# Kernel tuning notes

Measured on AMD Instinct MI355X. Metric: run time of the kernel, lower is better.

## Reference

```python
import jax, jax.numpy as jnp
import numpy as np

NUM_T = 1000      # diffusion timesteps
TIME_DIM = 16     # gaussian time embedding size
DIST_DIM = 16     # gaussian distance embedding size


def _gsmear(x, stop, num_g):
    # GaussianSmearing with linearly spaced centers in [0, stop]
    offsets = jnp.linspace(0.0, stop, num_g)
    coeff = -0.5 / (offsets[1] - offsets[0]) ** 2
    return jnp.exp(coeff * (x[:, None] - offsets[None, :]) ** 2)


def setup_inputs():
    key = jax.random.key(0)
    ks = jax.random.split(key, 20)
    N, EH, G = 20000, 100000, 1000          # nodes, halfedges, graphs
    NT, ND, ED, L, NE = 16, 256, 128, 2, 5   # node types, node_dim, edge_dim, blocks, edge types
    h_node = jax.nn.one_hot(jax.random.randint(ks[0], (N,), 0, NT), NT, dtype=jnp.float32)
    pos_node = jax.random.normal(ks[1], (N, 3), dtype=jnp.float32) * 3.0
    batch_node = jnp.sort(jax.random.randint(ks[2], (N,), 0, G))
    half = jax.random.randint(ks[3], (2, EH), 0, N)
    edge_index = jnp.concatenate([half, half[::-1]], axis=1)  # halfedges + flipped
    bh = jnp.sort(jax.random.randint(ks[4], (EH,), 0, G))
    batch_edge = jnp.concatenate([bh, bh], axis=0)
    t = jax.random.randint(ks[5], (G,), 0, NUM_T)

    def w(k, shape):
        fan_in = shape[-2] if len(shape) > 1 else shape[-1]
        return jax.random.normal(k, shape, dtype=jnp.float32) / np.sqrt(fan_in)

    e_in = ED + 2 * ND + DIST_DIM + 1
    return {
        'h_node': h_node, 'pos_node': pos_node, 'batch_node': batch_node,
        'edge_index': edge_index, 'batch_edge': batch_edge, 't': t,
        'W_node_emb': w(ks[6], (NT, ND - TIME_DIM)),
        'W_edge_emb': w(ks[7], (2 * NT, ED - TIME_DIM)),
        'We1': w(ks[8], (L, e_in, ED)), 'be1': jnp.zeros((L, ED), jnp.float32),
        'We2': w(ks[9], (L, ED, ED)), 'be2': jnp.zeros((L, ED), jnp.float32),
        'Wm': w(ks[10], (L, ND + ED, ND)), 'bm': jnp.zeros((L, ND), jnp.float32),
        'Wn1': w(ks[11], (L, 2 * ND + 1, ND)), 'bn1': jnp.zeros((L, ND), jnp.float32),
        'Wn2': w(ks[12], (L, ND, ND)), 'bn2': jnp.zeros((L, ND), jnp.float32),
        'Wd1': w(ks[13], (ED + ND, ED)), 'bd1': jnp.zeros((ED,), jnp.float32),
        'Wd2': w(ks[14], (ED, ED)), 'bd2': jnp.zeros((ED,), jnp.float32),
        'Wd3': w(ks[15], (ED, NE)), 'bd3': jnp.zeros((NE,), jnp.float32),
    }


def reference(h_node, pos_node, batch_node, edge_index, batch_edge, t,
              W_node_emb, W_edge_emb, We1, be1, We2, be2, Wm, bm,
              Wn1, bn1, Wn2, bn2, Wd1, bd1, Wd2, bd2, Wd3, bd3):
    src, dst = edge_index[0], edge_index[1]
    N = h_node.shape[0]
    L = We1.shape[0]

    # edge input features: concat of endpoint node features (gather)
    h_e0 = jnp.concatenate([h_node[src], h_node[dst]], axis=-1)

    tn = t[batch_node].astype(jnp.float32)  # per-node timestep
    te = t[batch_edge].astype(jnp.float32)  # per-edge timestep
    # linear embed + gaussian-smeared time embedding
    h_n = jnp.concatenate([h_node @ W_node_emb, _gsmear(tn, float(NUM_T), TIME_DIM)], axis=-1)
    h_e = jnp.concatenate([h_e0 @ W_edge_emb, _gsmear(te, float(NUM_T), TIME_DIM)], axis=-1)
    node_time = (tn / NUM_T)[:, None]
    edge_time = (te / NUM_T)[:, None]

    # geometric edge features
    d = jnp.linalg.norm(pos_node[dst] - pos_node[src], axis=-1)
    dist_emb = _gsmear(d, 10.0, DIST_DIM)

    # NodeEdgeNet: alternating edge / node residual updates
    for l in range(L):
        e_in = jnp.concatenate([h_e, h_n[src], h_n[dst], dist_emb, edge_time], axis=-1)
        h_e = h_e + jax.nn.relu(e_in @ We1[l] + be1[l]) @ We2[l] + be2[l]
        msg = jax.nn.relu(jnp.concatenate([h_n[src], h_e], axis=-1) @ Wm[l] + bm[l])
        agg = jax.ops.segment_sum(msg, dst, num_segments=N)
        n_in = jnp.concatenate([h_n, agg, node_time], axis=-1)
        h_n = h_n + jax.nn.relu(n_in @ Wn1[l] + bn1[l]) @ Wn2[l] + bn2[l]

    # symmetrize halfedges and decode edge types
    nh = h_e.shape[0] // 2
    h_ext = jnp.concatenate([h_e[:nh] + h_e[nh:],
                             h_n[src[:nh]] + h_n[dst[:nh]]], axis=-1)
    h = jax.nn.relu(h_ext @ Wd1 + bd1)
    h = jax.nn.relu(h @ Wd2 + bd2)
    return h @ Wd3 + bd3
```

## Files before the change

### kernel.cpp

```cpp
#include <hip/hip_runtime.h>
#include <math.h>


typedef __attribute__((ext_vector_type(8)))  short bf16x8;
typedef __attribute__((ext_vector_type(16))) float f32x16;

__device__ __forceinline__ float b2f(unsigned short u) {
    union { float f; unsigned int i; } x; x.i = ((unsigned int)u) << 16; return x.f;
}
__device__ __forceinline__ unsigned short f2b(float f) {
    union { float f; unsigned int i; } x; x.f = f;
    unsigned int r = x.i + 0x7fffu + ((x.i >> 16) & 1u);
    return (unsigned short)(r >> 16);
}
__device__ __forceinline__ bf16x8 ld8(const unsigned short* p) { return *(const bf16x8*)p; }
__device__ __forceinline__ bf16x8 zero8() { bf16x8 r = {0,0,0,0,0,0,0,0}; return r; }
__device__ __forceinline__ bf16x8 add8(bf16x8 a, bf16x8 b) {
    bf16x8 r;
#pragma unroll
    for (int j = 0; j < 8; j++) r[j] = (short)f2b(b2f((unsigned short)a[j]) + b2f((unsigned short)b[j]));
    return r;
}

#define MFMA4(ACC, A0, A1, B0, B1)                                                   \
    ACC[0][0] = __builtin_amdgcn_mfma_f32_32x32x16_bf16(A0, B0, ACC[0][0], 0, 0, 0); \
    ACC[0][1] = __builtin_amdgcn_mfma_f32_32x32x16_bf16(A0, B1, ACC[0][1], 0, 0, 0); \
    ACC[1][0] = __builtin_amdgcn_mfma_f32_32x32x16_bf16(A1, B0, ACC[1][0], 0, 0, 0); \
    ACC[1][1] = __builtin_amdgcn_mfma_f32_32x32x16_bf16(A1, B1, ACC[1][1], 0, 0, 0);

#define LANE_SETUP()                                  \
    const int tid  = threadIdx.x;                     \
    const int lane = tid & 63;                        \
    const int wave = tid >> 6;                        \
    const int wm = wave >> 1, wn = wave & 1;          \
    const int l31 = lane & 31, l5 = lane >> 5;        \
    (void)wm; (void)wn; (void)lane;

#define PIPELINE4(NITER, FETCH, ACC)                                  \
    {                                                                 \
        bf16x8 pa0[2], pb0[2], pa1[2], pb1[2], pa2[2], pb2[2];        \
        FETCH(0, pa0, pb0);                                           \
        if (1 < (NITER)) FETCH(1, pa1, pb1);                          \
        _Pragma("unroll")                                             \
        for (int i = 0; i < (NITER); i++) {                           \
            if (i + 2 < (NITER)) FETCH(i + 2, pa2, pb2);              \
            MFMA4(ACC, pa0[0], pa0[1], pb0[0], pb0[1]);               \
            pa0[0] = pa1[0]; pa0[1] = pa1[1];                         \
            pb0[0] = pb1[0]; pb0[1] = pb1[1];                         \
            pa1[0] = pa2[0]; pa1[1] = pa2[1];                         \
            pb1[0] = pb2[0]; pb1[1] = pb2[1];                         \
        }                                                             \
    }

#define PIPELINE2(NITER, FETCH, ACC)                                  \
    {                                                                 \
        bf16x8 pa0, pb0[2], pa1, pb1[2], pa2, pb2[2];                 \
        FETCH(0, pa0, pb0);                                           \
        if (1 < (NITER)) FETCH(1, pa1, pb1);                          \
        _Pragma("unroll")                                             \
        for (int i = 0; i < (NITER); i++) {                           \
            if (i + 2 < (NITER)) FETCH(i + 2, pa2, pb2);              \
            ACC[0] = __builtin_amdgcn_mfma_f32_32x32x16_bf16(pa0, pb0[0], ACC[0], 0, 0, 0); \
            ACC[1] = __builtin_amdgcn_mfma_f32_32x32x16_bf16(pa0, pb0[1], ACC[1], 0, 0, 0); \
            pa0 = pa1; pb0[0] = pb1[0]; pb0[1] = pb1[1];              \
            pa1 = pa2; pb1[0] = pb2[0]; pb1[1] = pb2[1];              \
        }                                                             \
    }

#define STAGED_COMPUTE(As, Bs, ACC)                                         \
    _Pragma("unroll")                                                       \
    for (int s = 0; s < 4; s++) {                                           \
        const int ks  = s * 2 + l5;                                         \
        const int ra0 = wm * 64 + l31, ra1 = ra0 + 32;                      \
        const int ca0 = wn * 64 + l31, ca1 = ca0 + 32;                      \
        bf16x8 a0 = *(const bf16x8*)&As[ra0][ks ^ (ra0 & 7)][0];            \
        bf16x8 a1 = *(const bf16x8*)&As[ra1][ks ^ (ra1 & 7)][0];            \
        bf16x8 b0 = *(const bf16x8*)&Bs[ca0][ks ^ (ca0 & 7)][0];            \
        bf16x8 b1 = *(const bf16x8*)&Bs[ca1][ks ^ (ca1 & 7)][0];            \
        MFMA4(ACC, a0, a1, b0, b1);                                         \
    }

__global__ void zero_i32_k(int* p, int n) {
    int i = blockIdx.x * 256 + threadIdx.x;
    if (i < n) p[i] = 0;
}
__global__ void hist_k(const int* __restrict__ dst, int* __restrict__ cnt, int E) {
    int e = blockIdx.x * 256 + threadIdx.x;
    if (e < E) atomicAdd(&cnt[dst[e]], 1);
}
__global__ __launch_bounds__(256) void scan_k(int* __restrict__ cnt, int N) {
    __shared__ int s[256];
    const int tidx  = threadIdx.x;
    const int chunk = (N + 255) / 256;
    const int lo = tidx * chunk;
    const int hi = (lo + chunk < N) ? lo + chunk : N;
    int sum = 0;
    for (int i = lo; i < hi; i++) sum += cnt[i];
    s[tidx] = sum;
    __syncthreads();
    for (int d = 1; d < 256; d <<= 1) {
        int t = (tidx >= d) ? s[tidx - d] : 0;
        __syncthreads();
        s[tidx] += t;
        __syncthreads();
    }
    int base = s[tidx] - sum;
    for (int i = lo; i < hi; i++) {
        int c = cnt[i];
        cnt[i] = base;
        base += c;
    }
}
__global__ void fill_k(const int* __restrict__ src, const int* __restrict__ dst,
                       const int* __restrict__ batch_edge, int* __restrict__ cur,
                       int* __restrict__ eids, int* __restrict__ pos,
                       int* __restrict__ srcp, int* __restrict__ dstp,
                       int* __restrict__ bep, int E) {
    int e = blockIdx.x * 256 + threadIdx.x;
    if (e < E) {
        int p = atomicAdd(&cur[dst[e]], 1);
        eids[p] = e;
        pos[e]  = p;
        srcp[p] = src[e];
        dstp[p] = dst[e];
        bep[p]  = batch_edge[e];
    }
}
__global__ void pad_k(int* eids, int* srcp, int* dstp, int* bep, int E, int Epad) {
    int i = E + blockIdx.x * 256 + threadIdx.x;
    if (i < Epad) { eids[i] = -1; srcp[i] = 0; dstp[i] = -1; bep[i] = 0; }
}

__global__ void typ_k(const float* __restrict__ h_node, int* __restrict__ typ, int N) {
    int i = blockIdx.x * 256 + threadIdx.x;
    if (i >= N) return;
    int ty = 0;
#pragma unroll
    for (int k = 0; k < 16; k++) if (h_node[i * 16 + k] > 0.5f) ty = k;
    typ[i] = ty;
}

struct TrDesc { const float* W; unsigned short* Wt; int K, N, Kpad; };
struct TrAll  { TrDesc d[14]; };

__global__ __launch_bounds__(256) void tr_all_k(TrAll a) {
    TrDesc t = a.d[blockIdx.y];
    int total = t.N * t.Kpad;
    for (int i = blockIdx.x * 256 + threadIdx.x; i < total; i += gridDim.x * 256) {
        int n = i / t.Kpad, k = i - n * t.Kpad;
        float v = (k < t.K) ? t.W[(size_t)k * t.N + n] : 0.f;
        t.Wt[(size_t)n * t.Kpad + k] = f2b(v);
    }
}

__global__ void tr_e1_k(const float* __restrict__ We1, unsigned short* __restrict__ Wt1e) {
    int idx = blockIdx.x * 256 + threadIdx.x;
    if (idx >= 128 * 192) return;
    int c = idx / 192, k = idx - c * 192;
    float v = 0.f;
    if (k < 128)      v = We1[(size_t)k * 128 + c];
    else if (k < 144) v = We1[(size_t)(640 + k - 128) * 128 + c];
    else if (k == 144) v = We1[(size_t)656 * 128 + c];
    Wt1e[idx] = f2b(v);
}

__global__ void embed_node_k(const int* __restrict__ typ,
                             const float* __restrict__ Wn,
                             const int* __restrict__ batch_node,
                             const int* __restrict__ t,
                             unsigned short* __restrict__ h_n, int N) {
    int idx = blockIdx.x * 256 + threadIdx.x;
    if (idx >= N * 32) return;
    int row = idx >> 5, seg = idx & 31;
    bf16x8 v;
    if (seg < 30) {
        const float* w = Wn + (size_t)typ[row] * 240 + seg * 8;
#pragma unroll
        for (int j = 0; j < 8; j++) v[j] = (short)f2b(w[j]);
    } else {
        float x = (float)t[batch_node[row]];
#pragma unroll
        for (int j = 0; j < 8; j++) {
            int col = seg * 8 + j;
            float dx = x - (1000.0f / 15.0f) * (float)(col - 240);
            v[j] = (short)f2b(expf(-1.125e-4f * dx * dx));
        }
    }
    *(bf16x8*)&h_n[(size_t)row * 256 + seg * 8] = v;
}

__global__ void embed_edge_k(const int* __restrict__ typ,
                             const float* __restrict__ We,
                             const int* __restrict__ srcp,
                             const int* __restrict__ dstp,
                             const int* __restrict__ bep,
                             const int* __restrict__ t,
                             unsigned short* __restrict__ h_e, int E) {
    int idx = blockIdx.x * 256 + threadIdx.x;
    if (idx >= E * 16) return;
    int row = idx >> 4, seg = idx & 15;
    bf16x8 v;
    if (seg < 14) {
        int d0 = dstp[row]; if (d0 < 0) d0 = 0;
        const float* ws = We + (size_t)typ[srcp[row]] * 112 + seg * 8;
        const float* wd = We + (size_t)(16 + typ[d0]) * 112 + seg * 8;
#pragma unroll
        for (int j = 0; j < 8; j++) v[j] = (short)f2b(ws[j] + wd[j]);
    } else {
        float x = (float)t[bep[row]];
#pragma unroll
        for (int j = 0; j < 8; j++) {
            int col = seg * 8 + j;
            float dx = x - (1000.0f / 15.0f) * (float)(col - 112);
            v[j] = (short)f2b(expf(-1.125e-4f * dx * dx));
        }
    }
    *(bf16x8*)&h_e[(size_t)row * 128 + seg * 8] = v;
}

__global__ __launch_bounds__(256) void proj_k(
    const unsigned short* __restrict__ h_n, const unsigned short* __restrict__ Wt,
    unsigned short* __restrict__ out, int N)
{
    LANE_SETUP();
    const int row0 = blockIdx.x * 64;
    const int col0 = blockIdx.y * 128;

    int rr = row0 + wm * 32 + l31;
    bool ok = rr < N;
    const unsigned short* hp = h_n + (size_t)(ok ? rr : 0) * 256;

    const unsigned short* Wa = Wt + (size_t)(col0 + wn * 64 + l31) * 256;
    const unsigned short* Wb = Wt + (size_t)(col0 + wn * 64 + 32 + l31) * 256;

    f32x16 acc[2] = {};
#define PJ_FETCH(i, A, B)                          \
    {                                              \
        const int c = 2 * (i) + l5;                \
        A = ok ? ld8(hp + (c << 3)) : zero8();     \
        B[0] = ld8(Wa + (c << 3));                 \
        B[1] = ld8(Wb + (c << 3));                 \
    }
    PIPELINE2(16, PJ_FETCH, acc)
#undef PJ_FETCH

#pragma unroll
    for (int nt = 0; nt < 2; nt++)
#pragma unroll
        for (int r2 = 0; r2 < 16; r2++) {
            int lrow = wm * 32 + (r2 & 3) + 8 * (r2 >> 2) + 4 * l5;
            int grow = row0 + lrow;
            if (grow >= N) continue;
            int col = col0 + wn * 64 + nt * 32 + l31;
            out[(size_t)grow * 256 + col] = f2b(acc[nt][r2]);
        }
}

__global__ __launch_bounds__(256) void edge_fused_k(
    unsigned short* __restrict__ h_e,
    const unsigned short* __restrict__ Wt1e, const float* __restrict__ be1,
    const unsigned short* __restrict__ Wt2, const float* __restrict__ be2,
    const unsigned short* __restrict__ P12,
    const float* __restrict__ pos, const int* __restrict__ srcp,
    const int* __restrict__ dstp, const int* __restrict__ t,
    const int* __restrict__ bep, int E)
{
    __shared__ __align__(16) char smem[128 * 136 * 2];
    unsigned short (*As)[8][8] = (unsigned short(*)[8][8])smem;
    unsigned short (*Bs)[8][8] = (unsigned short(*)[8][8])(smem + 16384);
    unsigned short (*H)[136]   = (unsigned short(*)[136])smem;

    LANE_SETUP();
    const int row0 = blockIdx.x * 128;
    const int srow = tid >> 3, sks = tid & 7;
    const int sx   = sks ^ (srow & 7);

    int rge[4], sg[4], dg[4]; bool okr[4];
#pragma unroll
    for (int p = 0; p < 4; p++) {
        int r = row0 + srow + p * 32;
        okr[p] = r < E;
        rge[p] = okr[p] ? r : 0;
        sg[p]  = srcp[rge[p]];
        dg[p]  = dstp[rge[p]]; if (dg[p] < 0) dg[p] = 0;
    }

#define EF_LOADA(KC, A)                                                        \
    {                                                                          \
        const int cg = (KC) * 8 + sks;                                         \
        _Pragma("unroll")                                                      \
        for (int p = 0; p < 4; p++) {                                          \
            bf16x8 v;                                                          \
            if (!okr[p] || cg >= 19) {                                         \
                v = zero8();                                                   \
            } else if (cg < 16) {                                              \
                v = ld8(h_e + (size_t)rge[p] * 128 + (cg << 3));               \
            } else if (cg < 18) {                                              \
                float dx = pos[dg[p] * 3 + 0] - pos[sg[p] * 3 + 0];            \
                float dy = pos[dg[p] * 3 + 1] - pos[sg[p] * 3 + 1];            \
                float dz = pos[dg[p] * 3 + 2] - pos[sg[p] * 3 + 2];            \
                float dist = sqrtf(dx * dx + dy * dy + dz * dz);               \
                _Pragma("unroll")                                              \
                for (int j = 0; j < 8; j++) {                                  \
                    float u = dist - (10.0f / 15.0f) * (float)((cg - 16) * 8 + j); \
                    v[j] = (short)f2b(expf(-1.125f * u * u));                  \
                }                                                              \
            } else {                                                           \
                v = zero8();                                                   \
                v[0] = (short)f2b((float)t[bep[rge[p]]] * 1e-3f);              \
            }                                                                  \
            A[p] = v;                                                          \
        }                                                                      \
    }
#define EF_LOADB(KC, B)                                                        \
    {                                                                          \
        const int cg = (KC) * 8 + sks;                                         \
        _Pragma("unroll")                                                      \
        for (int p = 0; p < 4; p++) {                                          \
            int col = srow + p * 32;                                           \
            B[p] = ld8(Wt1e + (size_t)col * 192 + (cg << 3));                  \
        }                                                                      \
    }

    f32x16 acc[2][2] = {};
    bf16x8 pA[4], pB[4], qA[4], qB[4];
    EF_LOADA(0, pA); EF_LOADB(0, pB);
    for (int kc = 0; kc < 3; kc++) {
#pragma unroll
        for (int p = 0; p < 4; p++) {
            *(bf16x8*)&As[srow + p * 32][sx][0] = pA[p];
            *(bf16x8*)&Bs[srow + p * 32][sx][0] = pB[p];
        }
        if (kc + 1 < 3) { EF_LOADA(kc + 1, qA); EF_LOADB(kc + 1, qB); }
        __syncthreads();
        STAGED_COMPUTE(As, Bs, acc);
        __syncthreads();
#pragma unroll
        for (int p = 0; p < 4; p++) { pA[p] = qA[p]; pB[p] = qB[p]; }
    }
#undef EF_LOADA
#undef EF_LOADB

#pragma unroll
    for (int mt = 0; mt < 2; mt++)
#pragma unroll
        for (int r = 0; r < 16; r++) {
            int lrow = wm * 64 + mt * 32 + (r & 3) + 8 * (r >> 2) + 4 * l5;
            int grow = row0 + lrow;
            bool ok = grow < E;
            int rg = ok ? grow : 0;
            int s = srcp[rg];
            int d = dstp[rg]; if (d < 0) d = 0;
            const unsigned short* p1 = P12 + (size_t)s * 256;
            const unsigned short* p2 = P12 + (size_t)d * 256 + 128;
#pragma unroll
            for (int nt = 0; nt < 2; nt++) {
                int col = wn * 64 + nt * 32 + l31;
                float v = acc[mt][nt][r] + be1[col] + b2f(p1[col]) + b2f(p2[col]);
                H[lrow][col] = f2b(fmaxf(v, 0.f));
            }
        }
    __syncthreads();

    const unsigned short* W2a = Wt2 + (size_t)(wn * 64 + l31) * 128;
    const unsigned short* W2b = Wt2 + (size_t)(wn * 64 + 32 + l31) * 128;
    f32x16 acc2[2][2] = {};
#define EF2_FETCH(i, A, B)                                          \
    {                                                               \
        const int c = 2 * (i) + l5;                                 \
        A[0] = *(const bf16x8*)&H[wm * 64 + l31][c << 3];           \
        A[1] = *(const bf16x8*)&H[wm * 64 + 32 + l31][c << 3];      \
        B[0] = ld8(W2a + (c << 3));                                 \
        B[1] = ld8(W2b + (c << 3));                                 \
    }
    PIPELINE4(8, EF2_FETCH, acc2)
#undef EF2_FETCH

#pragma unroll
    for (int mt = 0; mt < 2; mt++)
#pragma unroll
        for (int nt = 0; nt < 2; nt++)
#pragma unroll
            for (int r = 0; r < 16; r++) {
                int lrow = wm * 64 + mt * 32 + (r & 3) + 8 * (r >> 2) + 4 * l5;
                int grow = row0 + lrow;
                if (grow >= E) continue;
                int col = wn * 64 + nt * 32 + l31;
                size_t off = (size_t)grow * 128 + col;
                float v = acc2[mt][nt][r] + be2[col] + b2f(h_e[off]);
                h_e[off] = f2b(v);
            }
}

__global__ __launch_bounds__(256) void msg_k(
    const unsigned short* __restrict__ h_e, const unsigned short* __restrict__ h_n,
    const unsigned short* __restrict__ Wtm, const float* __restrict__ bm,
    const int* __restrict__ srcp, const int* __restrict__ dstp,
    float* __restrict__ agg, int E, int nRowTiles)
{
    __shared__ __align__(16) char smem[33024 + 512];
    unsigned short (*As)[8][8] = (unsigned short(*)[8][8])smem;
    unsigned short (*Bs)[8][8] = (unsigned short(*)[8][8])(smem + 16384);
    float (*T)[129] = (float(*)[129])smem;
    int* dstv = (int*)(smem + 33024);

    LANE_SETUP();
    const int b    = blockIdx.x;
    const int rowt = (b >> 4) * 8 + (b & 7);
    const int colh = (b >> 3) & 1;
    if (rowt >= nRowTiles) return;
    const int row0 = rowt * 128;
    const int col0 = colh * 128;

    if (tid < 128) dstv[tid] = dstp[row0 + tid];

    const int srow = tid >> 3, sks = tid & 7;
    const int sx   = sks ^ (srow & 7);

    const unsigned short *hns[4], *hep[4]; bool okr[4];
#pragma unroll
    for (int p = 0; p < 4; p++) {
        int r = row0 + srow + p * 32;
        okr[p] = r < E;
        int rg = okr[p] ? r : 0;
        hns[p] = h_n + (size_t)srcp[rg] * 256;
        hep[p] = h_e + (size_t)rg * 128;
    }

#define MSG_LOADA(KC, A)                                                 \
    {                                                                    \
        const int cg = (KC) * 8 + sks;                                   \
        _Pragma("unroll")                                                \
        for (int p = 0; p < 4; p++) {                                    \
            if (!okr[p])      A[p] = zero8();                            \
            else if (cg < 32) A[p] = ld8(hns[p] + (cg << 3));            \
            else              A[p] = ld8(hep[p] + ((cg - 32) << 3));     \
        }                                                                \
    }
#define MSG_LOADB(KC, B)                                                 \
    {                                                                    \
        const int cg = (KC) * 8 + sks;                                   \
        _Pragma("unroll")                                                \
        for (int p = 0; p < 4; p++) {                                    \
            int col = srow + p * 32;                                     \
            B[p] = ld8(Wtm + (size_t)(col0 + col) * 384 + (cg << 3));    \
        }                                                                \
    }

    f32x16 acc[2][2] = {};
    bf16x8 pA[4], pB[4], qA[4], qB[4];
    MSG_LOADA(0, pA); MSG_LOADB(0, pB);
    for (int kc = 0; kc < 6; kc++) {
#pragma unroll
        for (int p = 0; p < 4; p++) {
            *(bf16x8*)&As[srow + p * 32][sx][0] = pA[p];
            *(bf16x8*)&Bs[srow + p * 32][sx][0] = pB[p];
        }
        if (kc + 1 < 6) { MSG_LOADA(kc + 1, qA); MSG_LOADB(kc + 1, qB); }
        __syncthreads();
        STAGED_COMPUTE(As, Bs, acc);
        __syncthreads();
#pragma unroll
        for (int p = 0; p < 4; p++) { pA[p] = qA[p]; pB[p] = qB[p]; }
    }
#undef MSG_LOADA
#undef MSG_LOADB

    for (int ph = 0; ph < 2; ph++) {
        __syncthreads();
        if (wm == ph) {
#pragma unroll
            for (int mt = 0; mt < 2; mt++)
#pragma unroll
                for (int nt = 0; nt < 2; nt++)
#pragma unroll
                    for (int r = 0; r < 16; r++) {
                        int lrow = mt * 32 + (r & 3) + 8 * (r >> 2) + 4 * l5;
                        int col  = wn * 64 + nt * 32 + l31;
                        T[lrow][col] = acc[mt][nt][r] + bm[col0 + col];
                    }
        }
        __syncthreads();
        const int col = tid & 127, seg = tid >> 7;
        const int gcol = col0 + col;
        float run = 0.f; int prev = -1;
#pragma unroll 4
        for (int i = 0; i < 32; i++) {
            int lr = seg * 32 + i;
            int d  = dstv[ph * 64 + lr];
            float v = fmaxf(T[lr][col], 0.f);
            if (d != prev) {
                if (prev >= 0 && run != 0.f) atomicAdd(&agg[(size_t)prev * 256 + gcol], run);
                run = 0.f; prev = d;
            }
            if (d >= 0) run += v;
        }
        if (prev >= 0 && run != 0.f) atomicAdd(&agg[(size_t)prev * 256 + gcol], run);
    }
}

__global__ __launch_bounds__(256) void nin_k(
    const unsigned short* __restrict__ h_n, const float* __restrict__ agg,
    const unsigned short* __restrict__ Wtn1, const float* __restrict__ bn1,
    const int* __restrict__ batch_node, const int* __restrict__ t,
    unsigned short* __restrict__ Hn, int N)
{
    LANE_SETUP();
    const int row0 = blockIdx.x * 64;
    const int col0 = blockIdx.y * 128;

    int rr = row0 + wm * 32 + l31;
    bool ok = rr < N;
    int r = ok ? rr : 0;
    float timev = (float)t[batch_node[r]] * 1e-3f;
    const unsigned short* hp = h_n + (size_t)r * 256;
    const float*          ap = agg + (size_t)r * 256;

    const unsigned short* Wa = Wtn1 + (size_t)(col0 + wn * 64 + l31) * 544;
    const unsigned short* Wb = Wtn1 + (size_t)(col0 + wn * 64 + 32 + l31) * 544;

    f32x16 acc[2] = {};
#define NIN_FETCH(i, A, B)                                              \
    {                                                                   \
        const int c = 2 * (i) + l5;                                     \
        if (!ok) A = zero8();                                           \
        else if (c < 32) A = ld8(hp + (c << 3));                        \
        else if (c < 64) {                                              \
            const float* q = ap + ((c - 32) << 3);                      \
            bf16x8 v;                                                   \
            _Pragma("unroll")                                           \
            for (int j = 0; j < 8; j++) v[j] = (short)f2b(q[j]);        \
            A = v;                                                      \
        } else if (c == 64) { A = zero8(); A[0] = (short)f2b(timev); }  \
        else A = zero8();                                               \
        B[0] = ld8(Wa + (c << 3));                                      \
        B[1] = ld8(Wb + (c << 3));                                      \
    }
    PIPELINE2(34, NIN_FETCH, acc)
#undef NIN_FETCH

#pragma unroll
    for (int nt = 0; nt < 2; nt++)
#pragma unroll
        for (int r2 = 0; r2 < 16; r2++) {
            int lrow = wm * 32 + (r2 & 3) + 8 * (r2 >> 2) + 4 * l5;
            int grow = row0 + lrow;
            if (grow >= N) continue;
            int col = col0 + wn * 64 + nt * 32 + l31;
            float v = fmaxf(acc[nt][r2] + bn1[col], 0.f);
            Hn[(size_t)grow * 256 + col] = f2b(v);
        }
}

__global__ __launch_bounds__(256) void node_plain_k(
    const unsigned short* __restrict__ Hn, const unsigned short* __restrict__ Wtn2,
    const float* __restrict__ bn2, unsigned short* __restrict__ h_n, int N)
{
    LANE_SETUP();
    const int row0 = blockIdx.x * 64;
    const int col0 = blockIdx.y * 128;

    int rr = row0 + wm * 32 + l31;
    bool ok = rr < N;
    const unsigned short* hp = Hn + (size_t)(ok ? rr : 0) * 256;

    const unsigned short* Wa = Wtn2 + (size_t)(col0 + wn * 64 + l31) * 256;
    const unsigned short* Wb = Wtn2 + (size_t)(col0 + wn * 64 + 32 + l31) * 256;

    f32x16 acc[2] = {};
#define NP_FETCH(i, A, B)                          \
    {                                              \
        const int c = 2 * (i) + l5;                \
        A = ok ? ld8(hp + (c << 3)) : zero8();     \
        B[0] = ld8(Wa + (c << 3));                 \
        B[1] = ld8(Wb + (c << 3));                 \
    }
    PIPELINE2(16, NP_FETCH, acc)
#undef NP_FETCH

#pragma unroll
    for (int nt = 0; nt < 2; nt++)
#pragma unroll
        for (int r2 = 0; r2 < 16; r2++) {
            int lrow = wm * 32 + (r2 & 3) + 8 * (r2 >> 2) + 4 * l5;
            int grow = row0 + lrow;
            if (grow >= N) continue;
            int col = col0 + wn * 64 + nt * 32 + l31;
            size_t off = (size_t)grow * 256 + col;
            float v = acc[nt][r2] + bn2[col] + b2f(h_n[off]);
            h_n[off] = f2b(v);
        }
}

__global__ __launch_bounds__(256) void dec_fused_k(
    const unsigned short* __restrict__ h_e, const unsigned short* __restrict__ h_n,
    const unsigned short* __restrict__ Wtd1, const float* __restrict__ bd1,
    const unsigned short* __restrict__ Wtd2, const float* __restrict__ bd2,
    const float* __restrict__ Wd3, const float* __restrict__ bd3,
    const int* __restrict__ src, const int* __restrict__ dst,
    const int* __restrict__ pos, float* __restrict__ out, int nh)
{
    __shared__ __align__(16) char smem[128 * 136 * 2];
    __shared__ __align__(16) unsigned short H2[128][136];
    unsigned short (*As)[8][8] = (unsigned short(*)[8][8])smem;
    unsigned short (*Bs)[8][8] = (unsigned short(*)[8][8])(smem + 16384);
    unsigned short (*H1)[136]  = (unsigned short(*)[136])smem;

    LANE_SETUP();
    const int row0 = blockIdx.x * 128;
    const int srow = tid >> 3, sks = tid & 7;
    const int sx   = sks ^ (srow & 7);

    const unsigned short *pe1[4], *pe2[4], *pns[4], *pnd[4]; bool okr[4];
#pragma unroll
    for (int p = 0; p < 4; p++) {
        int r = row0 + srow + p * 32;
        okr[p] = r < nh;
        int rg = okr[p] ? r : 0;
        pe1[p] = h_e + (size_t)pos[rg] * 128;
        pe2[p] = h_e + (size_t)pos[rg + nh] * 128;
        pns[p] = h_n + (size_t)src[rg] * 256;
        pnd[p] = h_n + (size_t)dst[rg] * 256;
    }

#define DC_LOADA(KC, A)                                                              \
    {                                                                                \
        const int cg = (KC) * 8 + sks;                                               \
        _Pragma("unroll")                                                            \
        for (int p = 0; p < 4; p++) {                                                \
            if (!okr[p])      A[p] = zero8();                                        \
            else if (cg < 16) A[p] = add8(ld8(pe1[p] + (cg << 3)), ld8(pe2[p] + (cg << 3))); \
            else              A[p] = add8(ld8(pns[p] + ((cg - 16) << 3)), ld8(pnd[p] + ((cg - 16) << 3))); \
        }                                                                            \
    }
#define DC_LOADB(KC, B)                                                              \
    {                                                                                \
        const int cg = (KC) * 8 + sks;                                               \
        _Pragma("unroll")                                                            \
        for (int p = 0; p < 4; p++) {                                                \
            int col = srow + p * 32;                                                 \
            B[p] = ld8(Wtd1 + (size_t)col * 384 + (cg << 3));                        \
        }                                                                            \
    }

    f32x16 acc[2][2] = {};
    bf16x8 pA[4], pB[4], qA[4], qB[4];
    DC_LOADA(0, pA); DC_LOADB(0, pB);
    for (int kc = 0; kc < 6; kc++) {
#pragma unroll
        for (int p = 0; p < 4; p++) {
            *(bf16x8*)&As[srow + p * 32][sx][0] = pA[p];
            *(bf16x8*)&Bs[srow + p * 32][sx][0] = pB[p];
        }
        if (kc + 1 < 6) { DC_LOADA(kc + 1, qA); DC_LOADB(kc + 1, qB); }
        __syncthreads();
        STAGED_COMPUTE(As, Bs, acc);
        __syncthreads();
#pragma unroll
        for (int p = 0; p < 4; p++) { pA[p] = qA[p]; pB[p] = qB[p]; }
    }
#undef DC_LOADA
#undef DC_LOADB

#pragma unroll
    for (int mt = 0; mt < 2; mt++)
#pragma unroll
        for (int nt = 0; nt < 2; nt++)
#pragma unroll
            for (int r = 0; r < 16; r++) {
                int lrow = wm * 64 + mt * 32 + (r & 3) + 8 * (r >> 2) + 4 * l5;
                int col  = wn * 64 + nt * 32 + l31;
                H1[lrow][col] = f2b(fmaxf(acc[mt][nt][r] + bd1[col], 0.f));
            }
    __syncthreads();

    const unsigned short* W2a = Wtd2 + (size_t)(wn * 64 + l31) * 128;
    const unsigned short* W2b = Wtd2 + (size_t)(wn * 64 + 32 + l31) * 128;
    f32x16 acc2[2][2] = {};
#define DC2_FETCH(i, A, B)                                          \
    {                                                               \
        const int c = 2 * (i) + l5;                                 \
        A[0] = *(const bf16x8*)&H1[wm * 64 + l31][c << 3];          \
        A[1] = *(const bf16x8*)&H1[wm * 64 + 32 + l31][c << 3];     \
        B[0] = ld8(W2a + (c << 3));                                 \
        B[1] = ld8(W2b + (c << 3));                                 \
    }
    PIPELINE4(8, DC2_FETCH, acc2)
#undef DC2_FETCH

#pragma unroll
    for (int mt = 0; mt < 2; mt++)
#pragma unroll
        for (int nt = 0; nt < 2; nt++)
#pragma unroll
            for (int r = 0; r < 16; r++) {
                int lrow = wm * 64 + mt * 32 + (r & 3) + 8 * (r >> 2) + 4 * l5;
                int col  = wn * 64 + nt * 32 + l31;
                H2[lrow][col] = f2b(fmaxf(acc2[mt][nt][r] + bd2[col], 0.f));
            }
    __syncthreads();

    if (tid < 128) {
        int grow = row0 + tid;
        if (grow < nh) {
            float a5[5] = {0.f, 0.f, 0.f, 0.f, 0.f};
            for (int ks = 0; ks < 16; ks++) {
                bf16x8 hv = *(const bf16x8*)&H2[tid][ks << 3];
#pragma unroll
                for (int j = 0; j < 8; j++) {
                    float a = b2f((unsigned short)hv[j]);
                    int   k = ks * 8 + j;
#pragma unroll
                    for (int c5 = 0; c5 < 5; c5++) a5[c5] += a * Wd3[k * 5 + c5];
                }
            }
#pragma unroll
            for (int c5 = 0; c5 < 5; c5++) out[(size_t)grow * 5 + c5] = a5[c5] + bd3[c5];
        }
    }
}


__global__ void zero_k(float* p, long n) {
    long i = (long)blockIdx.x * 256 + threadIdx.x;
    if (i < n) p[i] = 0.f;
}


extern "C" void kernel_launch(void* const* d_in, const int* in_sizes, int n_in,
                              void* d_out, int out_size, void* d_ws, size_t ws_size,
                              hipStream_t stream) {
    const float* h_node     = (const float*)d_in[0];
    const float* pos_node   = (const float*)d_in[1];
    const int*   batch_node = (const int*)d_in[2];
    const int*   edge_index = (const int*)d_in[3];
    const int*   batch_edge = (const int*)d_in[4];
    const int*   t          = (const int*)d_in[5];
    const float* W_node_emb = (const float*)d_in[6];
    const float* W_edge_emb = (const float*)d_in[7];
    const float* We1 = (const float*)d_in[8];
    const float* be1 = (const float*)d_in[9];
    const float* We2 = (const float*)d_in[10];
    const float* be2 = (const float*)d_in[11];
    const float* Wm  = (const float*)d_in[12];
    const float* bm  = (const float*)d_in[13];
    const float* Wn1 = (const float*)d_in[14];
    const float* bn1 = (const float*)d_in[15];
    const float* Wn2 = (const float*)d_in[16];
    const float* bn2 = (const float*)d_in[17];
    const float* Wd1 = (const float*)d_in[18];
    const float* bd1 = (const float*)d_in[19];
    const float* Wd2 = (const float*)d_in[20];
    const float* bd2 = (const float*)d_in[21];
    const float* Wd3 = (const float*)d_in[22];
    const float* bd3 = (const float*)d_in[23];

    const int N  = in_sizes[0] / 16;
    const int E  = in_sizes[3] / 2;
    const int nh = E / 2;
    const int* src = edge_index;
    const int* dst = edge_index + E;

    const int gE   = (E + 127) / 128;
    const int gE8  = ((gE + 7) / 8) * 8;
    const int gN64 = (N + 63) / 64;
    const int Epad = gE * 128;

    float* agg  = (float*)d_ws;
    int*   cnt  = (int*)(agg + (size_t)N * 256);
    int*   eids = cnt + N;
    int*   pos  = eids + Epad;
    int*   srcp = pos + Epad;
    int*   dstp = srcp + Epad;
    int*   bep  = dstp + Epad;
    int*   typ  = bep + Epad;
    unsigned short* h_e = (unsigned short*)(typ + N);
    unsigned short* h_n = h_e + (size_t)E * 128;
    unsigned short* Hn  = h_n + (size_t)N * 256;
    unsigned short* P12 = Hn + (size_t)N * 256;
    unsigned short* Wt2  = P12 + (size_t)N * 256;
    unsigned short* Wtm  = Wt2 + 2 * 128 * 128;
    unsigned short* Wtn1 = Wtm + 2 * 256 * 384;
    unsigned short* Wtn2 = Wtn1 + 2 * 256 * 544;
    unsigned short* Wtd1 = Wtn2 + 2 * 256 * 256;
    unsigned short* Wtd2 = Wtd1 + 128 * 384;
    unsigned short* Wt1e = Wtd2 + 128 * 128;
    unsigned short* Wp12t = Wt1e + 2 * 128 * 192;

    zero_i32_k<<<(N + 255) / 256, 256, 0, stream>>>(cnt, N);
    hist_k<<<(E + 255) / 256, 256, 0, stream>>>(dst, cnt, E);
    scan_k<<<1, 256, 0, stream>>>(cnt, N);
    fill_k<<<(E + 255) / 256, 256, 0, stream>>>(src, dst, batch_edge, cnt,
                                                eids, pos, srcp, dstp, bep, E);
    if (Epad > E) pad_k<<<1, 256, 0, stream>>>(eids, srcp, dstp, bep, E, Epad);
    typ_k<<<(N + 255) / 256, 256, 0, stream>>>(h_node, typ, N);

    TrAll ta;
    for (int l = 0; l < 2; l++) {
        ta.d[l * 6 + 0] = { We2 + (size_t)l * 128 * 128, Wt2 + (size_t)l * 128 * 128, 128, 128, 128 };
        ta.d[l * 6 + 1] = { Wm  + (size_t)l * 384 * 256, Wtm + (size_t)l * 256 * 384, 384, 256, 384 };
        ta.d[l * 6 + 2] = { Wn1 + (size_t)l * 513 * 256, Wtn1 + (size_t)l * 256 * 544, 513, 256, 544 };
        ta.d[l * 6 + 3] = { Wn2 + (size_t)l * 256 * 256, Wtn2 + (size_t)l * 256 * 256, 256, 256, 256 };
        ta.d[l * 6 + 4] = { We1 + (size_t)l * 657 * 128 + 128 * 128,
                            Wp12t + (size_t)l * 256 * 256, 256, 128, 256 };
        ta.d[l * 6 + 5] = { We1 + (size_t)l * 657 * 128 + 384 * 128,
                            Wp12t + (size_t)l * 256 * 256 + 128 * 256, 256, 128, 256 };
    }
    ta.d[12] = { Wd1, Wtd1, 384, 128, 384 };
    ta.d[13] = { Wd2, Wtd2, 128, 128, 128 };
    tr_all_k<<<dim3(48, 14), 256, 0, stream>>>(ta);
    for (int l = 0; l < 2; l++)
        tr_e1_k<<<96, 256, 0, stream>>>(We1 + (size_t)l * 657 * 128, Wt1e + (size_t)l * 128 * 192);

    embed_node_k<<<(N * 32 + 255) / 256, 256, 0, stream>>>(typ, W_node_emb, batch_node, t, h_n, N);
    embed_edge_k<<<(E * 16 + 255) / 256, 256, 0, stream>>>(typ, W_edge_emb, srcp, dstp, bep, t, h_e, E);

    for (int l = 0; l < 2; l++) {
        proj_k<<<dim3(gN64, 2), 256, 0, stream>>>(h_n, Wp12t + (size_t)l * 256 * 256, P12, N);

        edge_fused_k<<<gE, 256, 0, stream>>>(
            h_e, Wt1e + (size_t)l * 128 * 192, be1 + l * 128,
            Wt2 + (size_t)l * 128 * 128, be2 + l * 128,
            P12, pos_node, srcp, dstp, t, bep, E);

        zero_k<<<(int)(((long)N * 256 + 255) / 256), 256, 0, stream>>>(agg, (long)N * 256);
        msg_k<<<gE8 * 2, 256, 0, stream>>>(
            h_e, h_n, Wtm + (size_t)l * 256 * 384, bm + l * 256, srcp, dstp, agg, E, gE);

        nin_k<<<dim3(gN64, 2), 256, 0, stream>>>(
            h_n, agg, Wtn1 + (size_t)l * 256 * 544, bn1 + l * 256, batch_node, t, Hn, N);

        node_plain_k<<<dim3(gN64, 2), 256, 0, stream>>>(
            Hn, Wtn2 + (size_t)l * 256 * 256, bn2 + l * 256, h_n, N);
    }

    dec_fused_k<<<(nh + 127) / 128, 256, 0, stream>>>(
        h_e, h_n, Wtd1, bd1, Wtd2, bd2, Wd3, bd3, src, dst, pos, (float*)d_out, nh);
}
```

Baseline: 834.2 us.

## Precompute per-node projections for message and decoder GEMMs instead of per-edge

The h_n[src] part of the message GEMM and the h_n[src]+h_n[dst] part of the decoder's first layer are now computed once per node by extending the node projection kernel. The edge kernels then gather those projected rows instead of raw node features. This shrinks the per-edge GEMM K dimension from 384 to 128 in both msg_k and dec_fused_k, trading edge-level FLOPs and gathers for node-level GEMMs. The cost is a wider projection buffer and an extra gather of a bf16 projected value in the epilogue, which adds bf16 rounding of the partial sums. Hn aliases P12Q and Pd aliases agg, so the buffer reuse order matters.

After: 1.064 ms. 27.6% more time.

```diff
diff --git a/kernel.cpp b/kernel.cpp
--- a/kernel.cpp
+++ b/kernel.cpp
@@ -141,7 +141,7 @@
 }
 
 struct TrDesc { const float* W; unsigned short* Wt; int K, N, Kpad; };
-struct TrAll  { TrDesc d[14]; };
+struct TrAll  { TrDesc d[17]; };
 
 __global__ __launch_bounds__(256) void tr_all_k(TrAll a) {
     TrDesc t = a.d[blockIdx.y];
@@ -220,7 +220,7 @@
 
 __global__ __launch_bounds__(256) void proj_k(
     const unsigned short* __restrict__ h_n, const unsigned short* __restrict__ Wt,
-    unsigned short* __restrict__ out, int N)
+    unsigned short* __restrict__ out, int OW, int N)
 {
     LANE_SETUP();
     const int row0 = blockIdx.x * 64;
@@ -252,7 +252,7 @@
             int grow = row0 + lrow;
             if (grow >= N) continue;
             int col = col0 + wn * 64 + nt * 32 + l31;
-            out[(size_t)grow * 256 + col] = f2b(acc[nt][r2]);
+            out[(size_t)grow * OW + col] = f2b(acc[nt][r2]);
         }
 }
 
@@ -351,8 +351,8 @@
             int rg = ok ? grow : 0;
             int s = srcp[rg];
             int d = dstp[rg]; if (d < 0) d = 0;
-            const unsigned short* p1 = P12 + (size_t)s * 256;
-            const unsigned short* p2 = P12 + (size_t)d * 256 + 128;
+            const unsigned short* p1 = P12 + (size_t)s * 512;
+            const unsigned short* p2 = P12 + (size_t)d * 512 + 128;
 #pragma unroll
             for (int nt = 0; nt < 2; nt++) {
                 int col = wn * 64 + nt * 32 + l31;
@@ -393,16 +393,17 @@
 }
 
 __global__ __launch_bounds__(256) void msg_k(
-    const unsigned short* __restrict__ h_e, const unsigned short* __restrict__ h_n,
-    const unsigned short* __restrict__ Wtm, const float* __restrict__ bm,
+    const unsigned short* __restrict__ h_e, const unsigned short* __restrict__ Q,
+    const unsigned short* __restrict__ Wtm_e, const float* __restrict__ bm,
     const int* __restrict__ srcp, const int* __restrict__ dstp,
     float* __restrict__ agg, int E, int nRowTiles)
 {
-    __shared__ __align__(16) char smem[33024 + 512];
+    __shared__ __align__(16) char smem[33024 + 1024];
     unsigned short (*As)[8][8] = (unsigned short(*)[8][8])smem;
     unsigned short (*Bs)[8][8] = (unsigned short(*)[8][8])(smem + 16384);
     float (*T)[129] = (float(*)[129])smem;
     int* dstv = (int*)(smem + 33024);
+    int* srcv = (int*)(smem + 33024 + 512);
 
     LANE_SETUP();
     const int b    = blockIdx.x;
@@ -412,30 +413,25 @@
     const int row0 = rowt * 128;
     const int col0 = colh * 128;
 
-    if (tid < 128) dstv[tid] = dstp[row0 + tid];
+    if (tid < 128) { dstv[tid] = dstp[row0 + tid]; srcv[tid] = srcp[row0 + tid]; }
 
     const int srow = tid >> 3, sks = tid & 7;
     const int sx   = sks ^ (srow & 7);
 
-    const unsigned short *hns[4], *hep[4]; bool okr[4];
+    const unsigned short* hep[4]; bool okr[4];
 #pragma unroll
     for (int p = 0; p < 4; p++) {
         int r = row0 + srow + p * 32;
         okr[p] = r < E;
-        int rg = okr[p] ? r : 0;
-        hns[p] = h_n + (size_t)srcp[rg] * 256;
-        hep[p] = h_e + (size_t)rg * 128;
+        hep[p] = h_e + (size_t)(okr[p] ? r : 0) * 128;
     }
 
 #define MSG_LOADA(KC, A)                                                 \
     {                                                                    \
         const int cg = (KC) * 8 + sks;                                   \
         _Pragma("unroll")                                                \
-        for (int p = 0; p < 4; p++) {                                    \
-            if (!okr[p])      A[p] = zero8();                            \
-            else if (cg < 32) A[p] = ld8(hns[p] + (cg << 3));            \
-            else              A[p] = ld8(hep[p] + ((cg - 32) << 3));     \
-        }                                                                \
+        for (int p = 0; p < 4; p++)                                      \
+            A[p] = okr[p] ? ld8(hep[p] + (cg << 3)) : zero8();           \
     }
 #define MSG_LOADB(KC, B)                                                 \
     {                                                                    \
@@ -443,20 +439,20 @@
         _Pragma("unroll")                                                \
         for (int p = 0; p < 4; p++) {                                    \
             int col = srow + p * 32;                                     \
-            B[p] = ld8(Wtm + (size_t)(col0 + col) * 384 + (cg << 3));    \
+            B[p] = ld8(Wtm_e + (size_t)(col0 + col) * 128 + (cg << 3));  \
         }                                                                \
     }
 
     f32x16 acc[2][2] = {};
     bf16x8 pA[4], pB[4], qA[4], qB[4];
     MSG_LOADA(0, pA); MSG_LOADB(0, pB);
-    for (int kc = 0; kc < 6; kc++) {
+    for (int kc = 0; kc < 2; kc++) {
 #pragma unroll
         for (int p = 0; p < 4; p++) {
             *(bf16x8*)&As[srow + p * 32][sx][0] = pA[p];
             *(bf16x8*)&Bs[srow + p * 32][sx][0] = pB[p];
         }
-        if (kc + 1 < 6) { MSG_LOADA(kc + 1, qA); MSG_LOADB(kc + 1, qB); }
+        if (kc + 1 < 2) { MSG_LOADA(kc + 1, qA); MSG_LOADB(kc + 1, qB); }
         __syncthreads();
         STAGED_COMPUTE(As, Bs, acc);
         __syncthreads();
@@ -488,7 +484,8 @@
         for (int i = 0; i < 32; i++) {
             int lr = seg * 32 + i;
             int d  = dstv[ph * 64 + lr];
-            float v = fmaxf(T[lr][col], 0.f);
+            int s  = srcv[ph * 64 + lr];
+            float v = fmaxf(T[lr][col] + b2f(Q[(size_t)s * 512 + 256 + gcol]), 0.f);
             if (d != prev) {
                 if (prev >= 0 && run != 0.f) atomicAdd(&agg[(size_t)prev * 256 + gcol], run);
                 run = 0.f; prev = d;
@@ -593,7 +590,7 @@
 }
 
 __global__ __launch_bounds__(256) void dec_fused_k(
-    const unsigned short* __restrict__ h_e, const unsigned short* __restrict__ h_n,
+    const unsigned short* __restrict__ h_e, const unsigned short* __restrict__ Pd,
     const unsigned short* __restrict__ Wtd1, const float* __restrict__ bd1,
     const unsigned short* __restrict__ Wtd2, const float* __restrict__ bd2,
     const float* __restrict__ Wd3, const float* __restrict__ bd3,
@@ -611,7 +608,7 @@
     const int srow = tid >> 3, sks = tid & 7;
     const int sx   = sks ^ (srow & 7);
 
-    const unsigned short *pe1[4], *pe2[4], *pns[4], *pnd[4]; bool okr[4];
+    const unsigned short *pe1[4], *pe2[4]; bool okr[4];
 #pragma unroll
     for (int p = 0; p < 4; p++) {
         int r = row0 + srow + p * 32;
@@ -619,19 +616,14 @@
         int rg = okr[p] ? r : 0;
         pe1[p] = h_e + (size_t)pos[rg] * 128;
         pe2[p] = h_e + (size_t)pos[rg + nh] * 128;
-        pns[p] = h_n + (size_t)src[rg] * 256;
-        pnd[p] = h_n + (size_t)dst[rg] * 256;
     }
 
 #define DC_LOADA(KC, A)                                                              \
     {                                                                                \
         const int cg = (KC) * 8 + sks;                                               \
         _Pragma("unroll")                                                            \
-        for (int p = 0; p < 4; p++) {                                                \
-            if (!okr[p])      A[p] = zero8();                                        \
-            else if (cg < 16) A[p] = add8(ld8(pe1[p] + (cg << 3)), ld8(pe2[p] + (cg << 3))); \
-            else              A[p] = add8(ld8(pns[p] + ((cg - 16) << 3)), ld8(pnd[p] + ((cg - 16) << 3))); \
-        }                                                                            \
+        for (int p = 0; p < 4; p++)                                                  \
+            A[p] = okr[p] ? add8(ld8(pe1[p] + (cg << 3)), ld8(pe2[p] + (cg << 3))) : zero8(); \
     }
 #define DC_LOADB(KC, B)                                                              \
     {                                                                                \
@@ -639,20 +631,20 @@
         _Pragma("unroll")                                                            \
         for (int p = 0; p < 4; p++) {                                                \
             int col = srow + p * 32;                                                 \
-            B[p] = ld8(Wtd1 + (size_t)col * 384 + (cg << 3));                        \
+            B[p] = ld8(Wtd1 + (size_t)col * 128 + (cg << 3));                        \
         }                                                                            \
     }
 
     f32x16 acc[2][2] = {};
     bf16x8 pA[4], pB[4], qA[4], qB[4];
     DC_LOADA(0, pA); DC_LOADB(0, pB);
-    for (int kc = 0; kc < 6; kc++) {
+    for (int kc = 0; kc < 2; kc++) {
 #pragma unroll
         for (int p = 0; p < 4; p++) {
             *(bf16x8*)&As[srow + p * 32][sx][0] = pA[p];
             *(bf16x8*)&Bs[srow + p * 32][sx][0] = pB[p];
         }
-        if (kc + 1 < 6) { DC_LOADA(kc + 1, qA); DC_LOADB(kc + 1, qB); }
+        if (kc + 1 < 2) { DC_LOADA(kc + 1, qA); DC_LOADB(kc + 1, qB); }
         __syncthreads();
         STAGED_COMPUTE(As, Bs, acc);
         __syncthreads();
@@ -665,13 +657,20 @@
 #pragma unroll
     for (int mt = 0; mt < 2; mt++)
 #pragma unroll
-        for (int nt = 0; nt < 2; nt++)
-#pragma unroll
-            for (int r = 0; r < 16; r++) {
-                int lrow = wm * 64 + mt * 32 + (r & 3) + 8 * (r >> 2) + 4 * l5;
-                int col  = wn * 64 + nt * 32 + l31;
-                H1[lrow][col] = f2b(fmaxf(acc[mt][nt][r] + bd1[col], 0.f));
+        for (int r = 0; r < 16; r++) {
+            int lrow = wm * 64 + mt * 32 + (r & 3) + 8 * (r >> 2) + 4 * l5;
+            int grow = row0 + lrow;
+            bool ok = grow < nh;
+            int rg = ok ? grow : 0;
+            const unsigned short* pd1 = Pd + (size_t)src[rg] * 128;
+            const unsigned short* pd2 = Pd + (size_t)dst[rg] * 128;
+#pragma unroll
+            for (int nt = 0; nt < 2; nt++) {
+                int col = wn * 64 + nt * 32 + l31;
+                float v = acc[mt][nt][r] + bd1[col] + b2f(pd1[col]) + b2f(pd2[col]);
+                H1[lrow][col] = f2b(fmaxf(v, 0.f));
             }
+        }
     __syncthreads();
 
     const unsigned short* W2a = Wtd2 + (size_t)(wn * 64 + l31) * 128;
@@ -774,18 +773,20 @@
     int*   dstp = srcp + Epad;
     int*   bep  = dstp + Epad;
     int*   typ  = bep + Epad;
-    unsigned short* h_e = (unsigned short*)(typ + N);
-    unsigned short* h_n = h_e + (size_t)E * 128;
-    unsigned short* Hn  = h_n + (size_t)N * 256;
-    unsigned short* P12 = Hn + (size_t)N * 256;
-    unsigned short* Wt2  = P12 + (size_t)N * 256;
-    unsigned short* Wtm  = Wt2 + 2 * 128 * 128;
-    unsigned short* Wtn1 = Wtm + 2 * 256 * 384;
-    unsigned short* Wtn2 = Wtn1 + 2 * 256 * 544;
-    unsigned short* Wtd1 = Wtn2 + 2 * 256 * 256;
-    unsigned short* Wtd2 = Wtd1 + 128 * 384;
-    unsigned short* Wt1e = Wtd2 + 128 * 128;
+    unsigned short* h_e  = (unsigned short*)(typ + N);
+    unsigned short* h_n  = h_e + (size_t)E * 128;
+    unsigned short* P12Q = h_n + (size_t)N * 256;
+    unsigned short* Hn   = P12Q;
+    unsigned short* Pd   = (unsigned short*)agg;
+    unsigned short* Wt2   = P12Q + (size_t)N * 512;
+    unsigned short* Wtn1  = Wt2 + 2 * 128 * 128;
+    unsigned short* Wtn2  = Wtn1 + 2 * 256 * 544;
+    unsigned short* Wt1e  = Wtn2 + 2 * 256 * 256;
     unsigned short* Wp12t = Wt1e + 2 * 128 * 192;
+    unsigned short* Wtm_e = Wp12t + 2 * 512 * 256;
+    unsigned short* Wtd1  = Wtm_e + 2 * 256 * 128;
+    unsigned short* Wtd2  = Wtd1 + 128 * 128;
+    unsigned short* Wpdt  = Wtd2 + 128 * 128;
 
     zero_i32_k<<<(N + 255) / 256, 256, 0, stream>>>(cnt, N);
     hist_k<<<(E + 255) / 256, 256, 0, stream>>>(dst, cnt, E);
@@ -797,18 +798,23 @@
 
     TrAll ta;
     for (int l = 0; l < 2; l++) {
-        ta.d[l * 6 + 0] = { We2 + (size_t)l * 128 * 128, Wt2 + (size_t)l * 128 * 128, 128, 128, 128 };
-        ta.d[l * 6 + 1] = { Wm  + (size_t)l * 384 * 256, Wtm + (size_t)l * 256 * 384, 384, 256, 384 };
-        ta.d[l * 6 + 2] = { Wn1 + (size_t)l * 513 * 256, Wtn1 + (size_t)l * 256 * 544, 513, 256, 544 };
-        ta.d[l * 6 + 3] = { Wn2 + (size_t)l * 256 * 256, Wtn2 + (size_t)l * 256 * 256, 256, 256, 256 };
-        ta.d[l * 6 + 4] = { We1 + (size_t)l * 657 * 128 + 128 * 128,
-                            Wp12t + (size_t)l * 256 * 256, 256, 128, 256 };
-        ta.d[l * 6 + 5] = { We1 + (size_t)l * 657 * 128 + 384 * 128,
-                            Wp12t + (size_t)l * 256 * 256 + 128 * 256, 256, 128, 256 };
-    }
-    ta.d[12] = { Wd1, Wtd1, 384, 128, 384 };
-    ta.d[13] = { Wd2, Wtd2, 128, 128, 128 };
-    tr_all_k<<<dim3(48, 14), 256, 0, stream>>>(ta);
+        int i = l * 7;
+        ta.d[i + 0] = { We2 + (size_t)l * 128 * 128, Wt2 + (size_t)l * 128 * 128, 128, 128, 128 };
+        ta.d[i + 1] = { Wn1 + (size_t)l * 513 * 256, Wtn1 + (size_t)l * 256 * 544, 513, 256, 544 };
+        ta.d[i + 2] = { Wn2 + (size_t)l * 256 * 256, Wtn2 + (size_t)l * 256 * 256, 256, 256, 256 };
+        ta.d[i + 3] = { We1 + (size_t)l * 657 * 128 + 128 * 128,
+                        Wp12t + (size_t)l * 512 * 256, 256, 128, 256 };
+        ta.d[i + 4] = { We1 + (size_t)l * 657 * 128 + 384 * 128,
+                        Wp12t + (size_t)l * 512 * 256 + 128 * 256, 256, 128, 256 };
+        ta.d[i + 5] = { Wm + (size_t)l * 384 * 256,
+                        Wp12t + (size_t)l * 512 * 256 + 256 * 256, 256, 256, 256 };
+        ta.d[i + 6] = { Wm + (size_t)l * 384 * 256 + 256 * 256,
+                        Wtm_e + (size_t)l * 256 * 128, 128, 256, 128 };
+    }
+    ta.d[14] = { Wd1, Wtd1, 128, 128, 128 };
+    ta.d[15] = { Wd2, Wtd2, 128, 128, 128 };
+    ta.d[16] = { Wd1 + 128 * 128, Wpdt, 256, 128, 256 };
+    tr_all_k<<<dim3(48, 17), 256, 0, stream>>>(ta);
     for (int l = 0; l < 2; l++)
         tr_e1_k<<<96, 256, 0, stream>>>(We1 + (size_t)l * 657 * 128, Wt1e + (size_t)l * 128 * 192);
 
@@ -816,16 +822,16 @@
     embed_edge_k<<<(E * 16 + 255) / 256, 256, 0, stream>>>(typ, W_edge_emb, srcp, dstp, bep, t, h_e, E);
 
     for (int l = 0; l < 2; l++) {
-        proj_k<<<dim3(gN64, 2), 256, 0, stream>>>(h_n, Wp12t + (size_t)l * 256 * 256, P12, N);
+        proj_k<<<dim3(gN64, 4), 256, 0, stream>>>(h_n, Wp12t + (size_t)l * 512 * 256, P12Q, 512, N);
 
         edge_fused_k<<<gE, 256, 0, stream>>>(
             h_e, Wt1e + (size_t)l * 128 * 192, be1 + l * 128,
             Wt2 + (size_t)l * 128 * 128, be2 + l * 128,
-            P12, pos_node, srcp, dstp, t, bep, E);
+            P12Q, pos_node, srcp, dstp, t, bep, E);
 
         zero_k<<<(int)(((long)N * 256 + 255) / 256), 256, 0, stream>>>(agg, (long)N * 256);
         msg_k<<<gE8 * 2, 256, 0, stream>>>(
-            h_e, h_n, Wtm + (size_t)l * 256 * 384, bm + l * 256, srcp, dstp, agg, E, gE);
+            h_e, P12Q, Wtm_e + (size_t)l * 256 * 128, bm + l * 256, srcp, dstp, agg, E, gE);
 
         nin_k<<<dim3(gN64, 2), 256, 0, stream>>>(
             h_n, agg, Wtn1 + (size_t)l * 256 * 544, bn1 + l * 256, batch_node, t, Hn, N);
@@ -834,6 +840,8 @@
             Hn, Wtn2 + (size_t)l * 256 * 256, bn2 + l * 256, h_n, N);
     }
 
+    proj_k<<<dim3(gN64, 1), 256, 0, stream>>>(h_n, Wpdt, Pd, 128, N);
+
     dec_fused_k<<<(nh + 127) / 128, 256, 0, stream>>>(
-        h_e, h_n, Wtd1, bd1, Wtd2, bd2, Wd3, bd3, src, dst, pos, (float*)d_out, nh);
-}
+        h_e, Pd, Wtd1, bd1, Wtd2, bd2, Wd3, bd3, src, dst, pos, (float*)d_out, nh);
+}
```
